# Optimization experiments

Hardware: AMD Instinct MI355X
Metric: run time of the kernel (lower is better)

The kernel has to match this reference:

```python
import jax, jax.numpy as jnp
import numpy as np

H_DIM = 64
GRID = 8
NBR = 2.0
BN_EPS = 1e-5
N_SEQ = 64
N_PED = 64
BOTTLENECK = 1024


def setup_inputs() -> dict:
    key = jax.random.key(0)
    k0, k1, k2, k3 = jax.random.split(key, 4)
    batch = N_SEQ * N_PED
    h_states = jax.random.normal(k0, (1, batch, H_DIM), jnp.float32)
    # positions spread over a 4x4 area so some neighbors fall inside the 2.0 neighborhood
    end_pos = jax.random.uniform(k1, (batch, 2), jnp.float32) * 4.0
    rel_pos = jax.random.normal(k2, (batch, 2), jnp.float32)
    starts = jnp.arange(N_SEQ, dtype=jnp.int32) * N_PED
    seq_start_end = jnp.stack([starts, starts + N_PED], axis=1)
    in_dim = GRID * GRID * H_DIM  # 4096
    W = jax.random.normal(k3, (in_dim, BOTTLENECK), jnp.float32) / np.sqrt(in_dim)
    b = jnp.zeros((BOTTLENECK,), jnp.float32)
    gamma = jnp.ones((BOTTLENECK,), jnp.float32)
    beta = jnp.zeros((BOTTLENECK,), jnp.float32)
    return {"h_states": h_states, "seq_start_end": seq_start_end, "end_pos": end_pos,
            "rel_pos": rel_pos, "W": W, "b": b, "gamma": gamma, "beta": beta}


def _pool_scene(hidden, pos):
    # hidden: (n, h), pos: (n, 2). Pair (i, j): ped j binned into ped i's grid.
    n, h = hidden.shape
    g2 = GRID * GRID
    half = NBR / 2.0
    tl_x = pos[:, 0] - half
    tl_y = pos[:, 1] + half
    br_x = pos[:, 0] + half
    br_y = pos[:, 1] - half
    px = pos[None, :, 0]  # (1, n) -> broadcast over i
    py = pos[None, :, 1]
    cell_x = jnp.floor((px - tl_x[:, None]) / NBR * GRID)
    cell_y = jnp.floor((tl_y[:, None] - py) / NBR * GRID)
    grid = (cell_x + cell_y * GRID).astype(jnp.int32) + 1  # slot 0 = trash bin
    oob = ((px >= br_x[:, None]) | (px <= tl_x[:, None]) |
           (py >= tl_y[:, None]) | (py <= br_y[:, None]) |
           jnp.eye(n, dtype=bool))  # self-interaction excluded
    grid = grid + (jnp.arange(n, dtype=jnp.int32) * g2)[:, None]
    grid = jnp.where(oob, 0, grid)  # (n, n)
    src = jnp.broadcast_to(hidden[None], (n, n, h)).reshape(-1, h)
    buf = jnp.zeros((n * g2 + 1, h), hidden.dtype).at[grid.reshape(-1)].add(src)
    return buf[1:].reshape(n, g2 * h)


def reference(h_states, seq_start_end, end_pos, rel_pos, W, b, gamma, beta):
    batch = end_pos.shape[0]
    n_seq = seq_start_end.shape[0]
    n_ped = batch // n_seq  # equal-length scenes by construction
    hid = h_states.reshape(-1, H_DIM).reshape(n_seq, n_ped, H_DIM)
    pos = end_pos.reshape(n_seq, n_ped, 2)
    pool_h = jax.vmap(_pool_scene)(hid, pos).reshape(batch, -1)  # (batch, 4096)
    x = pool_h @ W + b
    # BatchNorm1d in training mode (batch statistics, biased variance)
    mean = jnp.mean(x, axis=0)
    var = jnp.var(x, axis=0)
    x = (x - mean) * jax.lax.rsqrt(var + BN_EPS) * gamma + beta
    return jax.nn.relu(x)
```

## Files before the change

kernel.cpp:

```cpp
#include <hip/hip_runtime.h>
#include <hip/hip_bf16.h>


#define NPED  64
#define BATCH 4096
#define HDIM  64
#define G2    64
#define KDIM  4096
#define NOUT  1024

typedef __attribute__((ext_vector_type(8))) short short8;
typedef __attribute__((ext_vector_type(4))) float f32x4;

__device__ __forceinline__ unsigned short f2bf(float f) {
    __hip_bfloat16 h = __float2bfloat16(f);
    return *reinterpret_cast<unsigned short*>(&h);
}

__device__ __forceinline__ void lds_load16(const void* g, void* l) {
    __builtin_amdgcn_global_load_lds(
        (const __attribute__((address_space(1))) void*)g,
        (__attribute__((address_space(3))) void*)l, 16, 0, 0);
}

__global__ __launch_bounds__(128) void pool_kernel(const float* __restrict__ h,
                                                   const float* __restrict__ pos,
                                                   unsigned short* __restrict__ poolH) {
    __shared__ float acc[2][G2 * HDIM];
    __shared__ float pl[NPED * 2];
    int t = threadIdx.x;
    int w = t >> 6, lane = t & 63;
    int ped0 = blockIdx.x * 2;
    int sbase = ped0 & ~(NPED - 1);
    pl[t] = pos[sbase * 2 + t];
    #pragma unroll
    for (int c = 0; c < G2; ++c) acc[w][c * HDIM + lane] = 0.f;
    __syncthreads();

    int i = ped0 + w;
    int il = i & (NPED - 1);
    float cx0 = pl[2 * il], cy0 = pl[2 * il + 1];
    float tlx = cx0 - 1.f, tly = cy0 + 1.f, brx = cx0 + 1.f, bry = cy0 - 1.f;
    for (int j = 0; j < NPED; ++j) {
        if (j == il) continue;
        float px = pl[2 * j], py = pl[2 * j + 1];
        if (px >= brx || px <= tlx || py >= tly || py <= bry) continue;
        int cellx = (int)floorf((px - tlx) * 4.f);
        int celly = (int)floorf((tly - py) * 4.f);
        int cell = cellx + celly * 8;
        if ((unsigned)cell < 64u)
            acc[w][cell * HDIM + lane] += h[(size_t)(sbase + j) * HDIM + lane];
    }
    __syncthreads();
    unsigned int* out = (unsigned int*)poolH + (size_t)i * (KDIM / 2);
    #pragma unroll
    for (int p = 0; p < 32; ++p) {
        int lin = p * 64 + lane;
        unsigned int v = (unsigned int)f2bf(acc[w][2 * lin]) |
                         ((unsigned int)f2bf(acc[w][2 * lin + 1]) << 16);
        out[lin] = v;
    }
}

__global__ __launch_bounds__(256) void wt_kernel(const float* __restrict__ W,
                                                 unsigned short* __restrict__ Wt) {
    __shared__ unsigned short tile[64][66];
    int k0 = blockIdx.x * 64;
    int n0 = blockIdx.y * 64;
    int t = threadIdx.x;
    #pragma unroll
    for (int p = 0; p < 4; ++p) {
        int lin = p * 256 + t;
        int c4 = lin & 15, kl = lin >> 4;
        float4 v = ((const float4*)(W + (size_t)(k0 + kl) * NOUT + n0))[c4];
        tile[c4 * 4 + 0][kl] = f2bf(v.x);
        tile[c4 * 4 + 1][kl] = f2bf(v.y);
        tile[c4 * 4 + 2][kl] = f2bf(v.z);
        tile[c4 * 4 + 3][kl] = f2bf(v.w);
    }
    __syncthreads();
    unsigned int* out = (unsigned int*)Wt;
    #pragma unroll
    for (int p = 0; p < 8; ++p) {
        int lin = p * 256 + t;
        int ku = lin & 31, nl = lin >> 5;
        unsigned int v = (unsigned int)tile[nl][2 * ku] |
                         ((unsigned int)tile[nl][2 * ku + 1] << 16);
        out[(size_t)(n0 + nl) * (KDIM / 2) + (k0 >> 1) + ku] = v;
    }
}

__global__ __launch_bounds__(512) void gemm_kernel(const unsigned short* __restrict__ A,
                                                   const unsigned short* __restrict__ Bt,
                                                   float* __restrict__ C) {
    __shared__ __align__(16) unsigned short smem[4 * 128 * 64];
    int t = threadIdx.x;
    int w = t >> 6, lane = t & 63;
    int g = w >> 2;
    int wl = w & 3;
    int m0 = blockIdx.x * 128, n0 = blockIdx.y * 128;
    int wm = (wl >> 1) * 64, wn = (wl & 1) * 64;

    unsigned short* As = smem + g * 8192;
    unsigned short* Bs = smem + 16384 + g * 8192;

    f32x4 acc[4][4];
    #pragma unroll
    for (int i = 0; i < 4; ++i)
        #pragma unroll
        for (int j = 0; j < 4; ++j)
            acc[i][j] = (f32x4){0.f, 0.f, 0.f, 0.f};

    int rbase = wl * 32 + (lane >> 3);
    int koff = ((lane & 7) ^ (lane >> 3)) * 8;
    const unsigned short* Ag = A + (size_t)(m0 + rbase) * KDIM + g * 2048 + koff;
    const unsigned short* Bg = Bt + (size_t)(n0 + rbase) * KDIM + g * 2048 + koff;
    unsigned short* AsW = As + (wl * 4) * 512 + lane * 8;
    unsigned short* BsW = Bs + (wl * 4) * 512 + lane * 8;

    for (int kt = 0; kt < 2048; kt += 64) {
        #pragma unroll
        for (int q = 0; q < 4; ++q) {
            lds_load16(Ag + (size_t)q * 8 * KDIM + kt, AsW + q * 512);
            lds_load16(Bg + (size_t)q * 8 * KDIM + kt, BsW + q * 512);
        }
        __syncthreads();
        #pragma unroll
        for (int kk = 0; kk < 2; ++kk) {
            short8 af[4], bfr[4];
            int chunk = ((kk * 4 + (lane >> 4)) ^ (lane & 7)) * 8;
            #pragma unroll
            for (int i = 0; i < 4; ++i) {
                af[i]  = *(const short8*)&As[(wm + i * 16 + (lane & 15)) * 64 + chunk];
                bfr[i] = *(const short8*)&Bs[(wn + i * 16 + (lane & 15)) * 64 + chunk];
            }
            #pragma unroll
            for (int i = 0; i < 4; ++i)
                #pragma unroll
                for (int j = 0; j < 4; ++j)
                    acc[i][j] = __builtin_amdgcn_mfma_f32_16x16x32_bf16(af[i], bfr[j], acc[i][j], 0, 0, 0);
        }
        __syncthreads();
    }

    float* red = (float*)smem;
    int base2 = wl * 64 + lane;
    if (g == 1) {
        #pragma unroll
        for (int i = 0; i < 4; ++i)
            #pragma unroll
            for (int j = 0; j < 4; ++j)
                #pragma unroll
                for (int r = 0; r < 4; ++r)
                    red[(((i * 4 + j) * 4 + r) << 8) + base2] = acc[i][j][r];
    }
    __syncthreads();
    if (g == 0) {
        int col0 = n0 + wn + (lane & 15);
        int row0 = m0 + wm + ((lane >> 4) << 2);
        #pragma unroll
        for (int i = 0; i < 4; ++i)
            #pragma unroll
            for (int j = 0; j < 4; ++j)
                #pragma unroll
                for (int r = 0; r < 4; ++r) {
                    float v = acc[i][j][r] + red[(((i * 4 + j) * 4 + r) << 8) + base2];
                    C[(size_t)(row0 + i * 16 + r) * NOUT + col0 + j * 16] = v;
                }
    }
}

__global__ __launch_bounds__(256) void stats_kernel(const float* __restrict__ C,
                                                    float* __restrict__ stats) {
    int t = threadIdx.x;
    int colchunk = blockIdx.x & 3;
    int rowchunk = blockIdx.x >> 2;
    int col = colchunk * 256 + t;
    const float* p = C + (size_t)rowchunk * 32 * NOUT + col;
    float s = 0.f, s2 = 0.f;
    #pragma unroll 8
    for (int r = 0; r < 32; ++r) {
        float v = p[(size_t)r * NOUT];
        s += v; s2 += v * v;
    }
    atomicAdd(&stats[col], s);
    atomicAdd(&stats[NOUT + col], s2);
}

__global__ __launch_bounds__(256) void norm_kernel(float* __restrict__ C,
                                                   const float* __restrict__ stats,
                                                   const float* __restrict__ gamma,
                                                   const float* __restrict__ beta) {
    int idx = blockIdx.x * 256 + threadIdx.x;
    int col4 = idx & 255;
    float4 x = ((const float4*)C)[idx];
    float4 s = ((const float4*)stats)[col4];
    float4 q = ((const float4*)(stats + NOUT))[col4];
    float4 g = ((const float4*)gamma)[col4];
    float4 b = ((const float4*)beta)[col4];
    const float inv_n = 1.f / 4096.f;
    float m, inv;
    m = s.x * inv_n; inv = rsqrtf(q.x * inv_n - m * m + 1e-5f); x.x = fmaxf((x.x - m) * inv * g.x + b.x, 0.f);
    m = s.y * inv_n; inv = rsqrtf(q.y * inv_n - m * m + 1e-5f); x.y = fmaxf((x.y - m) * inv * g.y + b.y, 0.f);
    m = s.z * inv_n; inv = rsqrtf(q.z * inv_n - m * m + 1e-5f); x.z = fmaxf((x.z - m) * inv * g.z + b.z, 0.f);
    m = s.w * inv_n; inv = rsqrtf(q.w * inv_n - m * m + 1e-5f); x.w = fmaxf((x.w - m) * inv * g.w + b.w, 0.f);
    ((float4*)C)[idx] = x;
}

extern "C" void kernel_launch(void* const* d_in, const int* in_sizes, int n_in,
                              void* d_out, int out_size, void* d_ws, size_t ws_size,
                              hipStream_t stream) {
    const float* h      = (const float*)d_in[0];
    const float* endpos = (const float*)d_in[2];
    const float* W      = (const float*)d_in[4];
    const float* gamma  = (const float*)d_in[6];
    const float* beta   = (const float*)d_in[7];
    float* C = (float*)d_out;

    char* ws = (char*)d_ws;
    unsigned short* poolH = (unsigned short*)ws;
    unsigned short* Wt    = (unsigned short*)(ws + (size_t)BATCH * KDIM * 2);
    float* stats = (float*)(ws + (size_t)BATCH * KDIM * 2 + (size_t)NOUT * KDIM * 2);

    hipMemsetAsync(stats, 0, 2 * NOUT * sizeof(float), stream);
    pool_kernel<<<BATCH / 2, 128, 0, stream>>>(h, endpos, poolH);
    wt_kernel<<<dim3(KDIM / 64, NOUT / 64), 256, 0, stream>>>(W, Wt);
    gemm_kernel<<<dim3(BATCH / 128, NOUT / 128), 512, 0, stream>>>(poolH, Wt, C);
    stats_kernel<<<512, 256, 0, stream>>>(C, stats);
    norm_kernel<<<(BATCH * NOUT / 4) / 256, 256, 0, stream>>>(C, stats, gamma, beta);
}
```

Baseline: 179.1 us.

## Fuse BN stats into GEMM epilogue, double-buffer B, load A directly to registers

```diff
diff --git a/kernel.cpp b/kernel.cpp
--- a/kernel.cpp
+++ b/kernel.cpp
@@ -49,7 +49,7 @@
         int celly = (int)floorf((tly - py) * 4.f);
         int cell = cellx + celly * 8;
         if ((unsigned)cell < 64u)
-            acc[w][cell * HDIM + lane] += h[(size_t)(sbase + j) * HDIM + lane];
+            atomicAdd(&acc[w][cell * HDIM + lane], h[(size_t)(sbase + j) * HDIM + lane]);
     }
     __syncthreads();
     unsigned int* out = (unsigned int*)poolH + (size_t)i * (KDIM / 2);
@@ -63,11 +63,13 @@
 }
 
 __global__ __launch_bounds__(256) void wt_kernel(const float* __restrict__ W,
-                                                 unsigned short* __restrict__ Wt) {
+                                                 unsigned short* __restrict__ Wt,
+                                                 float* __restrict__ stats) {
     __shared__ unsigned short tile[64][66];
     int k0 = blockIdx.x * 64;
     int n0 = blockIdx.y * 64;
     int t = threadIdx.x;
+    if (blockIdx.x == 0 && blockIdx.y < 8) stats[blockIdx.y * 256 + t] = 0.f;
     #pragma unroll
     for (int p = 0; p < 4; ++p) {
         int lin = p * 256 + t;
@@ -92,7 +94,8 @@
 
 __global__ __launch_bounds__(512) void gemm_kernel(const unsigned short* __restrict__ A,
                                                    const unsigned short* __restrict__ Bt,
-                                                   float* __restrict__ C) {
+                                                   float* __restrict__ C,
+                                                   float* __restrict__ stats) {
     __shared__ __align__(16) unsigned short smem[4 * 128 * 64];
     int t = threadIdx.x;
     int w = t >> 6, lane = t & 63;
@@ -101,9 +104,6 @@
     int m0 = blockIdx.x * 128, n0 = blockIdx.y * 128;
     int wm = (wl >> 1) * 64, wn = (wl & 1) * 64;
 
-    unsigned short* As = smem + g * 8192;
-    unsigned short* Bs = smem + 16384 + g * 8192;
-
     f32x4 acc[4][4];
     #pragma unroll
     for (int i = 0; i < 4; ++i)
@@ -113,78 +113,111 @@
 
     int rbase = wl * 32 + (lane >> 3);
     int koff = ((lane & 7) ^ (lane >> 3)) * 8;
-    const unsigned short* Ag = A + (size_t)(m0 + rbase) * KDIM + g * 2048 + koff;
     const unsigned short* Bg = Bt + (size_t)(n0 + rbase) * KDIM + g * 2048 + koff;
-    unsigned short* AsW = As + (wl * 4) * 512 + lane * 8;
-    unsigned short* BsW = Bs + (wl * 4) * 512 + lane * 8;
-
-    for (int kt = 0; kt < 2048; kt += 64) {
-        #pragma unroll
-        for (int q = 0; q < 4; ++q) {
-            lds_load16(Ag + (size_t)q * 8 * KDIM + kt, AsW + q * 512);
-            lds_load16(Bg + (size_t)q * 8 * KDIM + kt, BsW + q * 512);
-        }
+    int ldsoff = (wl * 4) * 512 + lane * 8;
+
+    const unsigned short* Ap[4];
+    #pragma unroll
+    for (int i = 0; i < 4; ++i)
+        Ap[i] = A + (size_t)(m0 + wm + i * 16 + (lane & 15)) * KDIM
+                  + g * 2048 + (lane >> 4) * 8;
+
+    #pragma unroll
+    for (int q = 0; q < 4; ++q)
+        lds_load16(Bg, smem + (g * 2) * 8192 + ldsoff + q * 512),
+        Bg += (size_t)8 * KDIM;
+    Bg -= (size_t)32 * KDIM;
+
+    short8 afc[2][4], afn[2][4];
+    #pragma unroll
+    for (int kk = 0; kk < 2; ++kk)
+        #pragma unroll
+        for (int i = 0; i < 4; ++i)
+            afc[kk][i] = *(const short8*)(Ap[i] + kk * 32);
+
+    int buf = 0;
+    #pragma unroll 2
+    for (int j = 0; j < 32; ++j) {
+        int kt = j * 64;
         __syncthreads();
+        if (j + 1 < 32) {
+            int ktn = kt + 64;
+            #pragma unroll
+            for (int q = 0; q < 4; ++q)
+                lds_load16(Bg + (size_t)q * 8 * KDIM + ktn,
+                           smem + (g * 2 + (buf ^ 1)) * 8192 + ldsoff + q * 512);
+            #pragma unroll
+            for (int kk = 0; kk < 2; ++kk)
+                #pragma unroll
+                for (int i = 0; i < 4; ++i)
+                    afn[kk][i] = *(const short8*)(Ap[i] + ktn + kk * 32);
+        }
+        const unsigned short* Bs = smem + (g * 2 + buf) * 8192;
         #pragma unroll
         for (int kk = 0; kk < 2; ++kk) {
-            short8 af[4], bfr[4];
+            short8 bfr[4];
             int chunk = ((kk * 4 + (lane >> 4)) ^ (lane & 7)) * 8;
             #pragma unroll
-            for (int i = 0; i < 4; ++i) {
-                af[i]  = *(const short8*)&As[(wm + i * 16 + (lane & 15)) * 64 + chunk];
-                bfr[i] = *(const short8*)&Bs[(wn + i * 16 + (lane & 15)) * 64 + chunk];
-            }
+            for (int jj = 0; jj < 4; ++jj)
+                bfr[jj] = *(const short8*)&Bs[(wn + jj * 16 + (lane & 15)) * 64 + chunk];
             #pragma unroll
             for (int i = 0; i < 4; ++i)
                 #pragma unroll
-                for (int j = 0; j < 4; ++j)
-                    acc[i][j] = __builtin_amdgcn_mfma_f32_16x16x32_bf16(af[i], bfr[j], acc[i][j], 0, 0, 0);
-        }
-        __syncthreads();
+                for (int jj = 0; jj < 4; ++jj)
+                    acc[i][jj] = __builtin_amdgcn_mfma_f32_16x16x32_bf16(afc[kk][i], bfr[jj], acc[i][jj], 0, 0, 0);
+        }
+        if (j + 1 < 32) {
+            #pragma unroll
+            for (int kk = 0; kk < 2; ++kk)
+                #pragma unroll
+                for (int i = 0; i < 4; ++i)
+                    afc[kk][i] = afn[kk][i];
+        }
+        buf ^= 1;
     }
 
     float* red = (float*)smem;
     int base2 = wl * 64 + lane;
+    __syncthreads();
     if (g == 1) {
         #pragma unroll
         for (int i = 0; i < 4; ++i)
             #pragma unroll
-            for (int j = 0; j < 4; ++j)
+            for (int jj = 0; jj < 4; ++jj)
                 #pragma unroll
                 for (int r = 0; r < 4; ++r)
-                    red[(((i * 4 + j) * 4 + r) << 8) + base2] = acc[i][j][r];
+                    red[(((i * 4 + jj) * 4 + r) << 8) + base2] = acc[i][jj][r];
     }
     __syncthreads();
     if (g == 0) {
         int col0 = n0 + wn + (lane & 15);
         int row0 = m0 + wm + ((lane >> 4) << 2);
+        float s[4] = {0.f, 0.f, 0.f, 0.f}, s2[4] = {0.f, 0.f, 0.f, 0.f};
         #pragma unroll
         for (int i = 0; i < 4; ++i)
             #pragma unroll
-            for (int j = 0; j < 4; ++j)
+            for (int jj = 0; jj < 4; ++jj)
                 #pragma unroll
                 for (int r = 0; r < 4; ++r) {
-                    float v = acc[i][j][r] + red[(((i * 4 + j) * 4 + r) << 8) + base2];
-                    C[(size_t)(row0 + i * 16 + r) * NOUT + col0 + j * 16] = v;
+                    float v = acc[i][jj][r] + red[(((i * 4 + jj) * 4 + r) << 8) + base2];
+                    C[(size_t)(row0 + i * 16 + r) * NOUT + col0 + jj * 16] = v;
+                    s[jj] += v; s2[jj] += v * v;
                 }
-    }
-}
-
-__global__ __launch_bounds__(256) void stats_kernel(const float* __restrict__ C,
-                                                    float* __restrict__ stats) {
-    int t = threadIdx.x;
-    int colchunk = blockIdx.x & 3;
-    int rowchunk = blockIdx.x >> 2;
-    int col = colchunk * 256 + t;
-    const float* p = C + (size_t)rowchunk * 32 * NOUT + col;
-    float s = 0.f, s2 = 0.f;
-    #pragma unroll 8
-    for (int r = 0; r < 32; ++r) {
-        float v = p[(size_t)r * NOUT];
-        s += v; s2 += v * v;
-    }
-    atomicAdd(&stats[col], s);
-    atomicAdd(&stats[NOUT + col], s2);
+        #pragma unroll
+        for (int jj = 0; jj < 4; ++jj) {
+            s[jj]  += __shfl_xor(s[jj], 16, 64);
+            s[jj]  += __shfl_xor(s[jj], 32, 64);
+            s2[jj] += __shfl_xor(s2[jj], 16, 64);
+            s2[jj] += __shfl_xor(s2[jj], 32, 64);
+        }
+        if (lane < 16) {
+            #pragma unroll
+            for (int jj = 0; jj < 4; ++jj) {
+                atomicAdd(&stats[col0 + jj * 16], s[jj]);
+                atomicAdd(&stats[NOUT + col0 + jj * 16], s2[jj]);
+            }
+        }
+    }
 }
 
 __global__ __launch_bounds__(256) void norm_kernel(float* __restrict__ C,
@@ -222,10 +255,8 @@
     unsigned short* Wt    = (unsigned short*)(ws + (size_t)BATCH * KDIM * 2);
     float* stats = (float*)(ws + (size_t)BATCH * KDIM * 2 + (size_t)NOUT * KDIM * 2);
 
-    hipMemsetAsync(stats, 0, 2 * NOUT * sizeof(float), stream);
     pool_kernel<<<BATCH / 2, 128, 0, stream>>>(h, endpos, poolH);
-    wt_kernel<<<dim3(KDIM / 64, NOUT / 64), 256, 0, stream>>>(W, Wt);
-    gemm_kernel<<<dim3(BATCH / 128, NOUT / 128), 512, 0, stream>>>(poolH, Wt, C);
-    stats_kernel<<<512, 256, 0, stream>>>(C, stats);
+    wt_kernel<<<dim3(KDIM / 64, NOUT / 64), 256, 0, stream>>>(W, Wt, stats);
+    gemm_kernel<<<dim3(BATCH / 128, NOUT / 128), 512, 0, stream>>>(poolH, Wt, C, stats);
     norm_kernel<<<(BATCH * NOUT / 4) / 256, 256, 0, stream>>>(C, stats, gamma, beta);
 }
```

New measurement: 216.0 us. 1.21x slower.

## Split GEMM K across grid z, combine partials in stats kernel, drop memset

Applied to the files above, without the earlier changes.

```diff
diff --git a/kernel.cpp b/kernel.cpp
--- a/kernel.cpp
+++ b/kernel.cpp
@@ -49,7 +49,7 @@
         int celly = (int)floorf((tly - py) * 4.f);
         int cell = cellx + celly * 8;
         if ((unsigned)cell < 64u)
-            acc[w][cell * HDIM + lane] += h[(size_t)(sbase + j) * HDIM + lane];
+            atomicAdd(&acc[w][cell * HDIM + lane], h[(size_t)(sbase + j) * HDIM + lane]);
     }
     __syncthreads();
     unsigned int* out = (unsigned int*)poolH + (size_t)i * (KDIM / 2);
@@ -63,11 +63,13 @@
 }
 
 __global__ __launch_bounds__(256) void wt_kernel(const float* __restrict__ W,
-                                                 unsigned short* __restrict__ Wt) {
+                                                 unsigned short* __restrict__ Wt,
+                                                 float* __restrict__ stats) {
     __shared__ unsigned short tile[64][66];
     int k0 = blockIdx.x * 64;
     int n0 = blockIdx.y * 64;
     int t = threadIdx.x;
+    if (blockIdx.x == 0 && blockIdx.y < 8) stats[blockIdx.y * 256 + t] = 0.f;
     #pragma unroll
     for (int p = 0; p < 4; ++p) {
         int lin = p * 256 + t;
@@ -90,15 +92,17 @@
     }
 }
 
-__global__ __launch_bounds__(512) void gemm_kernel(const unsigned short* __restrict__ A,
-                                                   const unsigned short* __restrict__ Bt,
-                                                   float* __restrict__ C) {
+__global__ __launch_bounds__(512, 4) void gemm_kernel(const unsigned short* __restrict__ A,
+                                                      const unsigned short* __restrict__ Bt,
+                                                      float* __restrict__ C,
+                                                      float* __restrict__ P1) {
     __shared__ __align__(16) unsigned short smem[4 * 128 * 64];
     int t = threadIdx.x;
     int w = t >> 6, lane = t & 63;
     int g = w >> 2;
     int wl = w & 3;
     int m0 = blockIdx.x * 128, n0 = blockIdx.y * 128;
+    int kbase = blockIdx.z * 2048 + g * 1024;
     int wm = (wl >> 1) * 64, wn = (wl & 1) * 64;
 
     unsigned short* As = smem + g * 8192;
@@ -113,12 +117,12 @@
 
     int rbase = wl * 32 + (lane >> 3);
     int koff = ((lane & 7) ^ (lane >> 3)) * 8;
-    const unsigned short* Ag = A + (size_t)(m0 + rbase) * KDIM + g * 2048 + koff;
-    const unsigned short* Bg = Bt + (size_t)(n0 + rbase) * KDIM + g * 2048 + koff;
+    const unsigned short* Ag = A + (size_t)(m0 + rbase) * KDIM + kbase + koff;
+    const unsigned short* Bg = Bt + (size_t)(n0 + rbase) * KDIM + kbase + koff;
     unsigned short* AsW = As + (wl * 4) * 512 + lane * 8;
     unsigned short* BsW = Bs + (wl * 4) * 512 + lane * 8;
 
-    for (int kt = 0; kt < 2048; kt += 64) {
+    for (int kt = 0; kt < 1024; kt += 64) {
         #pragma unroll
         for (int q = 0; q < 4; ++q) {
             lds_load16(Ag + (size_t)q * 8 * KDIM + kt, AsW + q * 512);
@@ -156,6 +160,7 @@
     }
     __syncthreads();
     if (g == 0) {
+        float* dst = blockIdx.z ? P1 : C;
         int col0 = n0 + wn + (lane & 15);
         int row0 = m0 + wm + ((lane >> 4) << 2);
         #pragma unroll
@@ -165,22 +170,25 @@
                 #pragma unroll
                 for (int r = 0; r < 4; ++r) {
                     float v = acc[i][j][r] + red[(((i * 4 + j) * 4 + r) << 8) + base2];
-                    C[(size_t)(row0 + i * 16 + r) * NOUT + col0 + j * 16] = v;
+                    dst[(size_t)(row0 + i * 16 + r) * NOUT + col0 + j * 16] = v;
                 }
     }
 }
 
-__global__ __launch_bounds__(256) void stats_kernel(const float* __restrict__ C,
-                                                    float* __restrict__ stats) {
+__global__ __launch_bounds__(256) void combine_stats(float* __restrict__ C,
+                                                     const float* __restrict__ P1,
+                                                     float* __restrict__ stats) {
     int t = threadIdx.x;
     int colchunk = blockIdx.x & 3;
     int rowchunk = blockIdx.x >> 2;
     int col = colchunk * 256 + t;
-    const float* p = C + (size_t)rowchunk * 32 * NOUT + col;
+    size_t base = (size_t)rowchunk * 32 * NOUT + col;
     float s = 0.f, s2 = 0.f;
     #pragma unroll 8
     for (int r = 0; r < 32; ++r) {
-        float v = p[(size_t)r * NOUT];
+        size_t ix = base + (size_t)r * NOUT;
+        float v = C[ix] + P1[ix];
+        C[ix] = v;
         s += v; s2 += v * v;
     }
     atomicAdd(&stats[col], s);
@@ -220,12 +228,13 @@
     char* ws = (char*)d_ws;
     unsigned short* poolH = (unsigned short*)ws;
     unsigned short* Wt    = (unsigned short*)(ws + (size_t)BATCH * KDIM * 2);
-    float* stats = (float*)(ws + (size_t)BATCH * KDIM * 2 + (size_t)NOUT * KDIM * 2);
-
-    hipMemsetAsync(stats, 0, 2 * NOUT * sizeof(float), stream);
+    float* P1    = (float*)(ws + (size_t)BATCH * KDIM * 2 + (size_t)NOUT * KDIM * 2);
+    float* stats = (float*)(ws + (size_t)BATCH * KDIM * 2 + (size_t)NOUT * KDIM * 2
+                               + (size_t)BATCH * NOUT * 4);
+
     pool_kernel<<<BATCH / 2, 128, 0, stream>>>(h, endpos, poolH);
-    wt_kernel<<<dim3(KDIM / 64, NOUT / 64), 256, 0, stream>>>(W, Wt);
-    gemm_kernel<<<dim3(BATCH / 128, NOUT / 128), 512, 0, stream>>>(poolH, Wt, C);
-    stats_kernel<<<512, 256, 0, stream>>>(C, stats);
+    wt_kernel<<<dim3(KDIM / 64, NOUT / 64), 256, 0, stream>>>(W, Wt, stats);
+    gemm_kernel<<<dim3(BATCH / 128, NOUT / 128, 2), 512, 0, stream>>>(poolH, Wt, C, P1);
+    combine_stats<<<512, 256, 0, stream>>>(C, P1, stats);
     norm_kernel<<<(BATCH * NOUT / 4) / 256, 256, 0, stream>>>(C, stats, gamma, beta);
 }
```

Measured after the change: 184.8 us. 1.03x slower.
